# Kernel tuning notes

Hardware: AMD Instinct MI355X
Metric: run time of the kernel (lower is better)

Reference implementation:

```python
import jax, jax.numpy as jnp
import numpy as np

B, T_IN, F, NB = 32768, 3, 6, 10
H = 256
BD = H // 2            # baseline_dim
T_OUT = 5
DIN = F + H + BD       # decoder LSTMCell input size
EPS = 1e-5


def _lstm_cell(x, h, c, W_ih, W_hh, b_ih, b_hh):
    # PyTorch gate order: i, f, g, o
    z = x @ W_ih.T + h @ W_hh.T + b_ih + b_hh
    i, f, g, o = jnp.split(z, 4, axis=-1)
    c = jax.nn.sigmoid(f) * c + jax.nn.sigmoid(i) * jnp.tanh(g)
    h = jax.nn.sigmoid(o) * jnp.tanh(c)
    return h, c


def _lstm_layer(xs, W_ih, W_hh, b_ih, b_hh):
    # xs: (T, B, D_in) -> outputs (T, B, H), final (h, c)
    Bn = xs.shape[1]
    h0 = jnp.zeros((Bn, H), xs.dtype)
    c0 = jnp.zeros((Bn, H), xs.dtype)

    def step(carry, x):
        h, c = carry
        h, c = _lstm_cell(x, h, c, W_ih, W_hh, b_ih, b_hh)
        return (h, c), h

    (hT, cT), ys = jax.lax.scan(step, (h0, c0), xs)
    return ys, hT, cT


def setup_inputs() -> dict:
    key = jax.random.key(0)
    ks = jax.random.split(key, 16)
    s = 0.05
    d = {
        "cbc_input": jax.random.normal(ks[0], (B, T_IN, F), jnp.float32),
        "baseline": jax.random.normal(ks[1], (B, NB), jnp.float32),
        # encoder LSTM layer 0 / 1
        "W_ih0": jax.random.normal(ks[2], (4 * H, F), jnp.float32) * s,
        "W_hh0": jax.random.normal(ks[3], (4 * H, H), jnp.float32) * s,
        "b_ih0": jnp.zeros((4 * H,), jnp.float32),
        "b_hh0": jnp.zeros((4 * H,), jnp.float32),
        "W_ih1": jax.random.normal(ks[4], (4 * H, H), jnp.float32) * s,
        "W_hh1": jax.random.normal(ks[5], (4 * H, H), jnp.float32) * s,
        "b_ih1": jnp.zeros((4 * H,), jnp.float32),
        "b_hh1": jnp.zeros((4 * H,), jnp.float32),
        # baseline encoder: Linear + ReLU + LayerNorm
        "Wb": jax.random.normal(ks[6], (BD, NB), jnp.float32) * s,
        "bb": jnp.zeros((BD,), jnp.float32),
        "ln_g": jnp.ones((BD,), jnp.float32),
        "ln_b": jnp.zeros((BD,), jnp.float32),
        # Bahdanau attention
        "W1a": jax.random.normal(ks[7], (H, H), jnp.float32) * s,
        "b1a": jnp.zeros((H,), jnp.float32),
        "W2a": jax.random.normal(ks[8], (H, H), jnp.float32) * s,
        "b2a": jnp.zeros((H,), jnp.float32),
        "va": jax.random.normal(ks[9], (1, H), jnp.float32) * s,
        "ba": jnp.zeros((1,), jnp.float32),
        # decoder LSTMCell
        "Wd_ih": jax.random.normal(ks[10], (4 * H, DIN), jnp.float32) * s,
        "Wd_hh": jax.random.normal(ks[11], (4 * H, H), jnp.float32) * s,
        "bd_ih": jnp.zeros((4 * H,), jnp.float32),
        "bd_hh": jnp.zeros((4 * H,), jnp.float32),
        # output projection MLP
        "Wo1": jax.random.normal(ks[12], (BD, H), jnp.float32) * s,
        "bo1": jnp.zeros((BD,), jnp.float32),
        "Wo2": jax.random.normal(ks[13], (F, BD), jnp.float32) * s,
        "bo2": jnp.zeros((F,), jnp.float32),
    }
    return d


def reference(cbc_input, baseline, W_ih0, W_hh0, b_ih0, b_hh0,
              W_ih1, W_hh1, b_ih1, b_hh1, Wb, bb, ln_g, ln_b,
              W1a, b1a, W2a, b2a, va, ba,
              Wd_ih, Wd_hh, bd_ih, bd_hh, Wo1, bo1, Wo2, bo2):
    # ---- encoder (2-layer LSTM, batch_first; eval mode so no dropout) ----
    xs = jnp.swapaxes(cbc_input, 0, 1)                      # (T, B, F)
    y0, _, _ = _lstm_layer(xs, W_ih0, W_hh0, b_ih0, b_hh0)  # (T, B, H)
    y1, hT, cT = _lstm_layer(y0, W_ih1, W_hh1, b_ih1, b_hh1)
    encoder_outputs = jnp.swapaxes(y1, 0, 1)                # (B, T, H)

    # ---- baseline encoder: Linear -> ReLU -> LayerNorm ----
    z = jax.nn.relu(baseline @ Wb.T + bb)
    mu = jnp.mean(z, axis=-1, keepdims=True)
    var = jnp.mean((z - mu) ** 2, axis=-1, keepdims=True)
    baseline_repr = (z - mu) * jax.lax.rsqrt(var + EPS) * ln_g + ln_b  # (B, BD)

    enc_proj = encoder_outputs @ W2a.T + b2a                # (B, T, H) precomputed
    last_cbc0 = cbc_input[:, -1, :]                         # (B, F)

    def step(carry, _):
        h, c, last_cbc = carry
        # Bahdanau attention
        q = (h @ W1a.T + b1a)[:, None, :]                   # (B, 1, H)
        scores = jnp.tanh(q + enc_proj) @ va.T + ba         # (B, T, 1)
        weights = jax.nn.softmax(scores, axis=1)
        context = jnp.sum(weights * encoder_outputs, axis=1)  # (B, H)
        dec_in = jnp.concatenate([last_cbc, context, baseline_repr], axis=1)
        h, c = _lstm_cell(dec_in, h, c, Wd_ih, Wd_hh, bd_ih, bd_hh)
        delta = jax.nn.relu(h @ Wo1.T + bo1) @ Wo2.T + bo2
        pred = last_cbc + delta
        return (h, c, pred), pred

    _, preds = jax.lax.scan(step, (hT, cT, last_cbc0), None, length=T_OUT)
    return jnp.swapaxes(preds, 0, 1)                        # (B, 5, F)
```

## Files before the change

### kernel.cpp

```cpp
#include <hip/hip_runtime.h>

typedef unsigned short u16;
typedef __bf16 bf16x8 __attribute__((ext_vector_type(8)));
typedef float f32x4 __attribute__((ext_vector_type(4)));

#define BATCH 32768L

__device__ __forceinline__ u16 f2b(float f) {
  union { float f; unsigned int u; } v; v.f = f;
  unsigned int r = v.u + 0x7fffu + ((v.u >> 16) & 1u);
  return (u16)(r >> 16);
}
__device__ __forceinline__ float b2f(u16 h) {
  union { unsigned int u; float f; } v; v.u = ((unsigned int)h) << 16;
  return v.f;
}
__device__ __forceinline__ float rcpf(float x) { return __builtin_amdgcn_rcpf(x); }
__device__ __forceinline__ float sigf(float x) {
  return rcpf(1.f + __builtin_amdgcn_exp2f(-1.442695041f * x));
}
__device__ __forceinline__ float tanh_f(float x) {
  return 1.f - 2.f * rcpf(1.f + __builtin_amdgcn_exp2f(2.885390082f * x));
}

__device__ __forceinline__ void gload16(const void* g, void* l) {
  __builtin_amdgcn_global_load_lds((const __attribute__((address_space(1))) unsigned int*)g,
                                   (__attribute__((address_space(3))) unsigned int*)l,
                                   16, 0, 0);
}

struct PrepP {
  const float* s[9]; u16* d[9]; int sc[9]; int dc[9]; long n[9];
  const float* ba[3]; const float* bb_[3]; float* bo[3];
};

__global__ void prep_kernel(PrepP p, long cvtTotal, long total) {
  for (long i = (long)blockIdx.x * blockDim.x + threadIdx.x; i < total;
       i += (long)gridDim.x * blockDim.x) {
    if (i < cvtTotal) {
      long off = i; int sg = 0;
      while (off >= p.n[sg]) { off -= p.n[sg]; ++sg; }
      long r = off / p.dc[sg]; int c = (int)(off - r * p.dc[sg]);
      p.d[sg][off] = (c < p.sc[sg]) ? f2b(p.s[sg][r * (long)p.sc[sg] + c]) : (u16)0;
    } else {
      long j = i - cvtTotal; int sg = (int)(j >> 10); int k = (int)(j & 1023);
      p.bo[sg][k] = p.ba[sg][k] + p.bb_[sg][k];
    }
  }
}

template <int EPI, int NG, int REMAP>
__global__ __launch_bounds__(256, 3)
void mfma_gemm7(const u16* __restrict__ A1, long lda1, int K1,
                const u16* __restrict__ W1, int wld1,
                const u16* __restrict__ A2, long lda2, int K2,
                const u16* __restrict__ W2, int wld2,
                int gs, int ys, const float* __restrict__ bias,
                u16* __restrict__ out0, int ldo, int relu,
                const float* __restrict__ cprev, float* __restrict__ cout,
                u16* __restrict__ hout, int ldh)
{
  __shared__ u16 As[2][64 * 32];
  __shared__ u16 Bs[2][NG * 64 * 32];
  const int tid = threadIdx.x;
  const int l = tid & 63, w = tid >> 6;

  int row_blk, yb;
  if constexpr (REMAP) {
    const int vid = blockIdx.x;
    row_blk = (vid >> 5) * 8 + (vid & 7);
    yb = (vid >> 3) & 3;
  } else {
    row_blk = blockIdx.x;
    yb = blockIdx.y;
  }
  const long bm = (long)row_blk * 64;

  const int nch1 = K1 >> 5;
  const int nch2 = A2 ? (K2 >> 5) : 0;
  const int nt = nch1 + nch2;

  const int colb = l & 15, rq = l >> 4;

  f32x4 acc[4][NG];
  {
    float bw[NG];
#pragma unroll
    for (int g = 0; g < NG; ++g) bw[g] = bias[g * gs + yb * ys + w * 16 + colb];
#pragma unroll
    for (int rf = 0; rf < 4; ++rf)
#pragma unroll
      for (int g = 0; g < NG; ++g) acc[rf][g] = (f32x4){bw[g], bw[g], bw[g], bw[g]};
  }

  const int l4q = l >> 2;
  const int swzs = (((l & 3) - (l >> 3)) & 3) * 16;

  const char* pA;
  const char* pB[NG];
  auto initA = [&](const u16* A, long lda) {
    pA = (const char*)A + ((bm + w * 16 + l4q) * lda) * 2 + swzs;
  };
  auto initB = [&](const u16* W, int wld) {
#pragma unroll
    for (int c = 0; c < NG; ++c) {
      const int brow = (w * NG + c) * 16 + l4q;
      const long wrow = (long)(brow >> 6) * gs + (long)yb * ys + (brow & 63);
      pB[c] = (const char*)W + (wrow * (long)wld) * 2 + swzs;
    }
  };
  auto stage = [&](int buf) {
    gload16(pA, &As[buf][(w * 16) * 32]);
    pA += 64;
#pragma unroll
    for (int c = 0; c < NG; ++c) {
      gload16(pB[c], &Bs[buf][((w * NG + c) * 16) * 32]);
      pB[c] += 64;
    }
  };

  initA(A1, lda1);
  initB(W1, wld1);
  stage(0);

  const int rb = l & 15;
  const int koff = ((((l >> 4) + ((l & 15) >> 1)) & 3) * 8);
  int cur = 0;
  for (int ch = 0; ch < nt; ++ch) {
    __syncthreads();
    if (ch + 1 < nt) {
      if (A2 && ch + 1 == nch1) { initA(A2, lda2); initB(W2, wld2); }
      stage(cur ^ 1);
    }
    const u16* Ab = As[cur];
    const u16* Bb = Bs[cur];
    bf16x8 af[4];
#pragma unroll
    for (int rf = 0; rf < 4; ++rf)
      af[rf] = *(const bf16x8*)&Ab[(rf * 16 + rb) * 32 + koff];
#pragma unroll
    for (int g = 0; g < NG; ++g) {
      bf16x8 bfr = *(const bf16x8*)&Bb[(g * 64 + w * 16 + rb) * 32 + koff];
#pragma unroll
      for (int rf = 0; rf < 4; ++rf)
        acc[rf][g] = __builtin_amdgcn_mfma_f32_16x16x32_bf16(af[rf], bfr, acc[rf][g], 0, 0, 0);
    }
    cur ^= 1;
  }

  if constexpr (EPI == 0) {
#pragma unroll
    for (int g = 0; g < NG; ++g) {
      const int wrow = g * gs + yb * ys + w * 16 + colb;
#pragma unroll
      for (int rf = 0; rf < 4; ++rf) {
#pragma unroll
        for (int r = 0; r < 4; ++r) {
          float vv = acc[rf][g][r];
          if (relu) vv = fmaxf(vv, 0.f);
          out0[(bm + rf * 16 + rq * 4 + r) * (long)ldo + wrow] = f2b(vv);
        }
      }
    }
  } else {
    const int cb = yb * ys + w * 16 + colb;
#pragma unroll
    for (int rf = 0; rf < 4; ++rf) {
#pragma unroll
      for (int r = 0; r < 4; ++r) {
        const long row = bm + rf * 16 + rq * 4 + r;
        const float zi = acc[rf][0][r];
        const float zf = acc[rf][1][r];
        const float zg = acc[rf][2][r];
        const float zo = acc[rf][3][r];
        const float cp = cprev ? cprev[row * 256 + cb] : 0.f;
        const float cn = sigf(zf) * cp + sigf(zi) * tanh_f(zg);
        const float hn = sigf(zo) * tanh_f(cn);
        cout[row * 256 + cb] = cn;
        hout[row * (long)ldh + cb] = f2b(hn);
      }
    }
  }
}

__global__ __launch_bounds__(256)
void front_kernel(const float* __restrict__ cbc, const float* __restrict__ baseline,
                  const float* __restrict__ Wb, const float* __restrict__ bb,
                  const float* __restrict__ ln_g, const float* __restrict__ ln_b,
                  u16* __restrict__ dec_in, u16* __restrict__ xbf)
{
  __shared__ float wbs[1280];
  __shared__ float bbs[128], lgs[128], lbs[128];
  const int tid = threadIdx.x;
  for (int i = tid; i < 1280; i += 256) wbs[i] = Wb[i];
  if (tid < 128) { bbs[tid] = bb[tid]; lgs[tid] = ln_g[tid]; lbs[tid] = ln_b[tid]; }
  __syncthreads();
  const int l = tid & 63, w = tid >> 6;
  const long row = (long)blockIdx.x * 4 + w;
#pragma unroll
  for (int e = l; e < 96; e += 64) {
    const int t = e >> 5, c = e & 31;
    xbf[(row * 3 + t) * 32 + c] = (c < 6) ? f2b(cbc[row * 18 + t * 6 + c]) : (u16)0;
  }
  if (l < 6) dec_in[row * 416 + l] = f2b(cbc[row * 18 + 12 + l]);
  else if (l < 32) dec_in[row * 416 + 390 + (l - 6)] = 0;
  float bl[10];
#pragma unroll
  for (int k = 0; k < 10; ++k) bl[k] = baseline[row * 10 + k];
  const int c0 = l, c1 = l + 64;
  float z0 = bbs[c0], z1 = bbs[c1];
#pragma unroll
  for (int k = 0; k < 10; ++k) { z0 += bl[k] * wbs[c0 * 10 + k]; z1 += bl[k] * wbs[c1 * 10 + k]; }
  z0 = fmaxf(z0, 0.f); z1 = fmaxf(z1, 0.f);
  float s = z0 + z1, sq = z0 * z0 + z1 * z1;
#pragma unroll
  for (int m = 32; m; m >>= 1) { s += __shfl_xor(s, m); sq += __shfl_xor(sq, m); }
  const float mu = s * (1.f / 128.f);
  const float var = sq * (1.f / 128.f) - mu * mu;
  const float rs = rsqrtf(var + 1e-5f);
  dec_in[row * 416 + 262 + c0] = f2b((z0 - mu) * rs * lgs[c0] + lbs[c0]);
  dec_in[row * 416 + 262 + c1] = f2b((z1 - mu) * rs * lgs[c1] + lbs[c1]);
}

__global__ __launch_bounds__(256)
void attn_kernel(const u16* __restrict__ q, const u16* __restrict__ ep,
                 const u16* __restrict__ eo, const float* __restrict__ va,
                 const float* __restrict__ ba, u16* __restrict__ dec_in)
{
  const int tid = threadIdx.x;
  const int l = tid & 63, w = tid >> 6;
  const long row = (long)blockIdx.x * 4 + w;
  const int c = l * 4;
  float qv[4], vav[4];
  {
    ushort4 qu = *(const ushort4*)&q[row * 256 + c];
    qv[0] = b2f(qu.x); qv[1] = b2f(qu.y); qv[2] = b2f(qu.z); qv[3] = b2f(qu.w);
    float4 vv = *(const float4*)&va[c];
    vav[0] = vv.x; vav[1] = vv.y; vav[2] = vv.z; vav[3] = vv.w;
  }
  float s[3];
#pragma unroll
  for (int t = 0; t < 3; ++t) {
    ushort4 eu = *(const ushort4*)&ep[row * 768 + t * 256 + c];
    float p = tanh_f(qv[0] + b2f(eu.x)) * vav[0]
            + tanh_f(qv[1] + b2f(eu.y)) * vav[1]
            + tanh_f(qv[2] + b2f(eu.z)) * vav[2]
            + tanh_f(qv[3] + b2f(eu.w)) * vav[3];
#pragma unroll
    for (int m = 32; m; m >>= 1) p += __shfl_xor(p, m);
    s[t] = p + ba[0];
  }
  const float mx = fmaxf(s[0], fmaxf(s[1], s[2]));
  const float e0 = __expf(s[0] - mx), e1 = __expf(s[1] - mx), e2 = __expf(s[2] - mx);
  const float inv = rcpf(e0 + e1 + e2);
  const float w0 = e0 * inv, w1 = e1 * inv, w2 = e2 * inv;
  const ushort4 a0 = *(const ushort4*)&eo[row * 768 + 0 * 256 + c];
  const ushort4 a1 = *(const ushort4*)&eo[row * 768 + 1 * 256 + c];
  const ushort4 a2 = *(const ushort4*)&eo[row * 768 + 2 * 256 + c];
  u16* dp = &dec_in[row * 416 + 6 + c];
  dp[0] = f2b(w0 * b2f(a0.x) + w1 * b2f(a1.x) + w2 * b2f(a2.x));
  dp[1] = f2b(w0 * b2f(a0.y) + w1 * b2f(a1.y) + w2 * b2f(a2.y));
  dp[2] = f2b(w0 * b2f(a0.z) + w1 * b2f(a1.z) + w2 * b2f(a2.z));
  dp[3] = f2b(w0 * b2f(a0.w) + w1 * b2f(a1.w) + w2 * b2f(a2.w));
}

__global__ __launch_bounds__(256)
void delta_kernel(const u16* __restrict__ t1, const float* __restrict__ Wo2,
                  const float* __restrict__ bo2, const float* __restrict__ lastp, int lstride,
                  float* __restrict__ outp, int ostride, u16* __restrict__ dec_in)
{
  __shared__ float w2s[768];
  __shared__ float part[64][4][6];
  const int tid = threadIdx.x;
  for (int i = tid; i < 768; i += 256) w2s[i] = Wo2[i];
  __syncthreads();
  const int rw = tid >> 2, q = tid & 3;
  const long row = (long)blockIdx.x * 64 + rw;
  float p[6] = {0.f, 0.f, 0.f, 0.f, 0.f, 0.f};
  const u16* tp = &t1[row * 128 + q * 32];
#pragma unroll
  for (int it = 0; it < 4; ++it) {
    int4 chunk = *(const int4*)&tp[it * 8];
    const u16* cu = (const u16*)&chunk;
#pragma unroll
    for (int e = 0; e < 8; ++e) {
      const float tv = b2f(cu[e]);
      const int k = q * 32 + it * 8 + e;
#pragma unroll
      for (int j = 0; j < 6; ++j) p[j] += tv * w2s[j * 128 + k];
    }
  }
#pragma unroll
  for (int j = 0; j < 6; ++j) part[rw][q][j] = p[j];
  __syncthreads();
  if (tid < 64) {
    const long r2 = (long)blockIdx.x * 64 + tid;
#pragma unroll
    for (int j = 0; j < 6; ++j) {
      const float d = bo2[j] + part[tid][0][j] + part[tid][1][j] + part[tid][2][j] + part[tid][3][j];
      const float pr = lastp[r2 * lstride + j] + d;
      outp[r2 * ostride + j] = pr;
      dec_in[r2 * 416 + j] = f2b(pr);
    }
  }
}

extern "C" void kernel_launch(void* const* d_in, const int* in_sizes, int n_in,
                              void* d_out, int out_size, void* d_ws, size_t ws_size,
                              hipStream_t stream) {
  const float* cbc   = (const float*)d_in[0];
  const float* base  = (const float*)d_in[1];
  const float* W_ih0 = (const float*)d_in[2];
  const float* W_hh0 = (const float*)d_in[3];
  const float* b_ih0 = (const float*)d_in[4];
  const float* b_hh0 = (const float*)d_in[5];
  const float* W_ih1 = (const float*)d_in[6];
  const float* W_hh1 = (const float*)d_in[7];
  const float* b_ih1 = (const float*)d_in[8];
  const float* b_hh1 = (const float*)d_in[9];
  const float* Wb    = (const float*)d_in[10];
  const float* bb    = (const float*)d_in[11];
  const float* ln_g  = (const float*)d_in[12];
  const float* ln_b  = (const float*)d_in[13];
  const float* W1a   = (const float*)d_in[14];
  const float* b1a   = (const float*)d_in[15];
  const float* W2a   = (const float*)d_in[16];
  const float* b2a   = (const float*)d_in[17];
  const float* va    = (const float*)d_in[18];
  const float* ba    = (const float*)d_in[19];
  const float* Wd_ih = (const float*)d_in[20];
  const float* Wd_hh = (const float*)d_in[21];
  const float* bd_ih = (const float*)d_in[22];
  const float* bd_hh = (const float*)d_in[23];
  const float* Wo1   = (const float*)d_in[24];
  const float* bo1   = (const float*)d_in[25];
  const float* Wo2   = (const float*)d_in[26];
  const float* bo2   = (const float*)d_in[27];
  float* out = (float*)d_out;
  (void)in_sizes; (void)n_in; (void)out_size;

  unsigned char* wsb = (unsigned char*)d_ws;
  size_t off = 0;
  auto alloc = [&](size_t bytes) -> void* {
    void* p = wsb + off;
    off += (bytes + 255) & ~(size_t)255;
    return p;
  };
  u16* wih0b = (u16*)alloc(1024 * 32 * 2);
  u16* whh0b = (u16*)alloc(1024 * 256 * 2);
  u16* wih1b = (u16*)alloc(1024 * 256 * 2);
  u16* whh1b = (u16*)alloc(1024 * 256 * 2);
  u16* wdihb = (u16*)alloc(1024 * 416 * 2);
  u16* wdhhb = (u16*)alloc(1024 * 256 * 2);
  u16* w1ab  = (u16*)alloc(256 * 256 * 2);
  u16* w2ab  = (u16*)alloc(256 * 256 * 2);
  u16* wo1b  = (u16*)alloc(128 * 256 * 2);
  float* bsum0 = (float*)alloc(1024 * 4);
  float* bsum1 = (float*)alloc(1024 * 4);
  float* bsumd = (float*)alloc(1024 * 4);

  const long perRow = 6656;
  long avail = (long)ws_size - (long)off - 32768;
  long R = avail > 0 ? avail / perRow : 512;
  R &= ~511L;
  if (R > BATCH) R = BATCH;
  if (R < 512) R = 512;

  u16* xbf    = (u16*)alloc((size_t)R * 96 * 2);
  u16* y0     = (u16*)alloc((size_t)R * 768 * 2);
  u16* y1     = (u16*)alloc((size_t)R * 768 * 2);
  float* cbuf = (float*)alloc((size_t)R * 256 * 4);
  u16* hdec0  = (u16*)alloc((size_t)R * 256 * 2);
  u16* hdec1  = (u16*)alloc((size_t)R * 256 * 2);
  u16* qt1    = (u16*)alloc((size_t)R * 256 * 2);
  u16* dec_in = (u16*)alloc((size_t)R * 416 * 2);

  {
    PrepP p;
    const float* ss[9] = {W_ih0, W_hh0, W_ih1, W_hh1, Wd_ih, Wd_hh, W1a, W2a, Wo1};
    u16* dd[9]         = {wih0b, whh0b, wih1b, whh1b, wdihb, wdhhb, w1ab, w2ab, wo1b};
    int scv[9]         = {6, 256, 256, 256, 390, 256, 256, 256, 256};
    int dcv[9]         = {32, 256, 256, 256, 416, 256, 256, 256, 256};
    long rows[9]       = {1024, 1024, 1024, 1024, 1024, 1024, 256, 256, 128};
    long cvtTotal = 0;
    for (int i = 0; i < 9; ++i) {
      p.s[i] = ss[i]; p.d[i] = dd[i]; p.sc[i] = scv[i]; p.dc[i] = dcv[i];
      p.n[i] = rows[i] * dcv[i]; cvtTotal += p.n[i];
    }
    p.ba[0] = b_ih0; p.bb_[0] = b_hh0; p.bo[0] = bsum0;
    p.ba[1] = b_ih1; p.bb_[1] = b_hh1; p.bo[1] = bsum1;
    p.ba[2] = bd_ih; p.bb_[2] = bd_hh; p.bo[2] = bsumd;
    prep_kernel<<<dim3(2048), dim3(256), 0, stream>>>(p, cvtTotal, cvtTotal + 3072);
  }

  const dim3 blk(256);

  for (long r0 = 0; r0 < BATCH; r0 += R) {
    const long Rc = (BATCH - r0 < R) ? (BATCH - r0) : R;
    const unsigned nb = (unsigned)(Rc / 64);
    const dim3 gcell(nb * 4);
    const float* cbc_c  = cbc + r0 * 18;
    const float* base_c = base + r0 * 10;
    float* out_c = out + r0 * 30;

    front_kernel<<<dim3((unsigned)(Rc / 4)), blk, 0, stream>>>(
        cbc_c, base_c, Wb, bb, ln_g, ln_b, dec_in, xbf);

    for (int t = 0; t < 3; ++t) {
      const u16* a2 = t ? (y0 + (t - 1) * 256) : nullptr;
      mfma_gemm7<1, 4, 1><<<gcell, blk, 0, stream>>>(
          xbf + t * 32, 96, 32, wih0b, 32,
          a2, 768, 256, whh0b, 256,
          256, 64, bsum0,
          nullptr, 0, 0,
          (t ? cbuf : nullptr), cbuf, y0 + t * 256, 768);
    }
    for (int t = 0; t < 3; ++t) {
      const u16* a2 = t ? (y1 + (t - 1) * 256) : nullptr;
      mfma_gemm7<1, 4, 1><<<gcell, blk, 0, stream>>>(
          y0 + t * 256, 768, 256, wih1b, 256,
          a2, 768, 256, whh1b, 256,
          256, 64, bsum1,
          nullptr, 0, 0,
          (t ? cbuf : nullptr), cbuf, y1 + t * 256, 768);
    }
    mfma_gemm7<0, 4, 0><<<dim3(nb * 3, 1), blk, 0, stream>>>(
        y1, 256, 256, w2ab, 256,
        nullptr, 0, 0, nullptr, 0,
        64, 0, b2a,
        y0, 256, 0,
        nullptr, nullptr, nullptr, 0);

    const u16* hcur = y1 + 2 * 256; long hld = 768;
    for (int s = 0; s < 5; ++s) {
      mfma_gemm7<0, 4, 0><<<dim3(nb, 1), blk, 0, stream>>>(
          hcur, hld, 256, w1ab, 256,
          nullptr, 0, 0, nullptr, 0,
          64, 0, b1a,
          qt1, 256, 0,
          nullptr, nullptr, nullptr, 0);
      attn_kernel<<<dim3((unsigned)(Rc / 4)), blk, 0, stream>>>(qt1, y0, y1, va, ba, dec_in);
      u16* hnext = (s & 1) ? hdec1 : hdec0;
      mfma_gemm7<1, 4, 1><<<gcell, blk, 0, stream>>>(
          dec_in, 416, 416, wdihb, 416,
          hcur, hld, 256, wdhhb, 256,
          256, 64, bsumd,
          nullptr, 0, 0,
          cbuf, cbuf, hnext, 256);
      hcur = hnext; hld = 256;
      mfma_gemm7<0, 2, 0><<<dim3(nb, 1), blk, 0, stream>>>(
          hcur, 256, 256, wo1b, 256,
          nullptr, 0, 0, nullptr, 0,
          64, 0, bo1,
          qt1, 128, 1,
          nullptr, nullptr, nullptr, 0);
      const float* lastp = (s == 0) ? (cbc_c + 12) : (out_c + (long)(s - 1) * 6);
      const int lstr = (s == 0) ? 18 : 30;
      delta_kernel<<<dim3((unsigned)(Rc / 64)), blk, 0, stream>>>(
          qt1, Wo2, bo2, lastp, lstr, out_c + (long)s * 6, 30, dec_in);
    }
  }
}
```

Before: 927.9 us.

## Deepen GEMM load pipeline with triple-buffered A tiles and partial vmcnt waits

The bf16 MFMA GEMM main loop now triple-buffers the A tile and double-buffers B. The A load is issued two chunks ahead and the B load one chunk ahead. The full __syncthreads is replaced by an explicit s_waitcnt vmcnt(1)/s_barrier, so the most recent A prefetch can stay in flight across the barrier. The MFMA block is also wrapped in s_setprio to favour math issue. Shared memory grows by one A buffer, and correctness now relies on hand-counted outstanding global loads.

Result: slower. 998.5 us (+7.6%).

```diff
diff --git a/kernel.cpp b/kernel.cpp
--- a/kernel.cpp
+++ b/kernel.cpp
@@ -51,7 +51,7 @@
 
 template <int EPI, int NG, int REMAP>
 __global__ __launch_bounds__(256, 3)
-void mfma_gemm7(const u16* __restrict__ A1, long lda1, int K1,
+void mfma_gemm8(const u16* __restrict__ A1, long lda1, int K1,
                 const u16* __restrict__ W1, int wld1,
                 const u16* __restrict__ A2, long lda2, int K2,
                 const u16* __restrict__ W2, int wld2,
@@ -60,7 +60,7 @@
                 const float* __restrict__ cprev, float* __restrict__ cout,
                 u16* __restrict__ hout, int ldh)
 {
-  __shared__ u16 As[2][64 * 32];
+  __shared__ u16 As[3][64 * 32];
   __shared__ u16 Bs[2][NG * 64 * 32];
   const int tid = threadIdx.x;
   const int l = tid & 63, w = tid >> 6;
@@ -109,9 +109,13 @@
       pB[c] = (const char*)W + (wrow * (long)wld) * 2 + swzs;
     }
   };
-  auto stage = [&](int buf) {
+  auto stageA = [&](int s, int buf) {
+    if (A2 && s == nch1) initA(A2, lda2);
     gload16(pA, &As[buf][(w * 16) * 32]);
     pA += 64;
+  };
+  auto stageB = [&](int s, int buf) {
+    if (A2 && s == nch1) initB(W2, wld2);
 #pragma unroll
     for (int c = 0; c < NG; ++c) {
       gload16(pB[c], &Bs[buf][((w * NG + c) * 16) * 32]);
@@ -121,23 +125,31 @@
 
   initA(A1, lda1);
   initB(W1, wld1);
-  stage(0);
+  stageA(0, 0);
+  stageB(0, 0);
+  if (nt > 1) stageA(1, 1);
 
   const int rb = l & 15;
   const int koff = ((((l >> 4) + ((l & 15) >> 1)) & 3) * 8);
-  int cur = 0;
+  int bA = 0, bB = 0;
   for (int ch = 0; ch < nt; ++ch) {
-    __syncthreads();
     if (ch + 1 < nt) {
-      if (A2 && ch + 1 == nch1) { initA(A2, lda2); initB(W2, wld2); }
-      stage(cur ^ 1);
-    }
-    const u16* Ab = As[cur];
-    const u16* Bb = Bs[cur];
+      asm volatile("s_waitcnt vmcnt(1)\n\ts_barrier" ::: "memory");
+    } else {
+      asm volatile("s_waitcnt vmcnt(0)\n\ts_barrier" ::: "memory");
+    }
+    if (ch + 1 < nt) stageB(ch + 1, bB ^ 1);
+    if (ch + 2 < nt) {
+      int nxt = bA + 2; if (nxt >= 3) nxt -= 3;
+      stageA(ch + 2, nxt);
+    }
+    const u16* Ab = As[bA];
+    const u16* Bb = Bs[bB];
     bf16x8 af[4];
 #pragma unroll
     for (int rf = 0; rf < 4; ++rf)
       af[rf] = *(const bf16x8*)&Ab[(rf * 16 + rb) * 32 + koff];
+    __builtin_amdgcn_s_setprio(1);
 #pragma unroll
     for (int g = 0; g < NG; ++g) {
       bf16x8 bfr = *(const bf16x8*)&Bb[(g * 64 + w * 16 + rb) * 32 + koff];
@@ -145,7 +157,9 @@
       for (int rf = 0; rf < 4; ++rf)
         acc[rf][g] = __builtin_amdgcn_mfma_f32_16x16x32_bf16(af[rf], bfr, acc[rf][g], 0, 0, 0);
     }
-    cur ^= 1;
+    __builtin_amdgcn_s_setprio(0);
+    bA = (bA + 1 == 3) ? 0 : bA + 1;
+    bB ^= 1;
   }
 
   if constexpr (EPI == 0) {
@@ -408,7 +422,7 @@
 
     for (int t = 0; t < 3; ++t) {
       const u16* a2 = t ? (y0 + (t - 1) * 256) : nullptr;
-      mfma_gemm7<1, 4, 1><<<gcell, blk, 0, stream>>>(
+      mfma_gemm8<1, 4, 1><<<gcell, blk, 0, stream>>>(
           xbf + t * 32, 96, 32, wih0b, 32,
           a2, 768, 256, whh0b, 256,
           256, 64, bsum0,
@@ -417,14 +431,14 @@
     }
     for (int t = 0; t < 3; ++t) {
       const u16* a2 = t ? (y1 + (t - 1) * 256) : nullptr;
-      mfma_gemm7<1, 4, 1><<<gcell, blk, 0, stream>>>(
+      mfma_gemm8<1, 4, 1><<<gcell, blk, 0, stream>>>(
           y0 + t * 256, 768, 256, wih1b, 256,
           a2, 768, 256, whh1b, 256,
           256, 64, bsum1,
           nullptr, 0, 0,
           (t ? cbuf : nullptr), cbuf, y1 + t * 256, 768);
     }
-    mfma_gemm7<0, 4, 0><<<dim3(nb * 3, 1), blk, 0, stream>>>(
+    mfma_gemm8<0, 4, 0><<<dim3(nb * 3, 1), blk, 0, stream>>>(
         y1, 256, 256, w2ab, 256,
         nullptr, 0, 0, nullptr, 0,
         64, 0, b2a,
@@ -433,7 +447,7 @@
 
     const u16* hcur = y1 + 2 * 256; long hld = 768;
     for (int s = 0; s < 5; ++s) {
-      mfma_gemm7<0, 4, 0><<<dim3(nb, 1), blk, 0, stream>>>(
+      mfma_gemm8<0, 4, 0><<<dim3(nb, 1), blk, 0, stream>>>(
           hcur, hld, 256, w1ab, 256,
           nullptr, 0, 0, nullptr, 0,
           64, 0, b1a,
@@ -441,14 +455,14 @@
           nullptr, nullptr, nullptr, 0);
       attn_kernel<<<dim3((unsigned)(Rc / 4)), blk, 0, stream>>>(qt1, y0, y1, va, ba, dec_in);
       u16* hnext = (s & 1) ? hdec1 : hdec0;
-      mfma_gemm7<1, 4, 1><<<gcell, blk, 0, stream>>>(
+      mfma_gemm8<1, 4, 1><<<gcell, blk, 0, stream>>>(
           dec_in, 416, 416, wdihb, 416,
           hcur, hld, 256, wdhhb, 256,
           256, 64, bsumd,
           nullptr, 0, 0,
           cbuf, cbuf, hnext, 256);
       hcur = hnext; hld = 256;
-      mfma_gemm7<0, 2, 0><<<dim3(nb, 1), blk, 0, stream>>>(
+      mfma_gemm8<0, 2, 0><<<dim3(nb, 1), blk, 0, stream>>>(
           hcur, 256, 256, wo1b, 256,
           nullptr, 0, 0, nullptr, 0,
           64, 0, bo1,
```

## Fuse query GEMM with attention and output MLP with delta in decoder

Applied to the files above, without the earlier changes.

Per decoder step, the W1a query projection GEMM is merged with the attention/softmax/context kernel, and the Wo1 ReLU GEMM is merged with the Wo2 delta/prediction kernel. Each fused kernel keeps its GEMM tile in LDS instead of writing it to global memory and reading it back, and it removes two launches per step. The cell GEMMs also get a templated min-waves launch bound, raised to 4. The cost is larger LDS use per block in the fused kernels, lower occupancy (launch bound of 2), and attention now handles only 64 rows per block with each wave walking 16 rows serially.

Result: faster. 881.6 us (-5.0%).

```diff
diff --git a/kernel.cpp b/kernel.cpp
--- a/kernel.cpp
+++ b/kernel.cpp
@@ -49,8 +49,8 @@
   }
 }
 
-template <int EPI, int NG, int REMAP>
-__global__ __launch_bounds__(256, 3)
+template <int EPI, int NG, int REMAP, int MINW>
+__global__ __launch_bounds__(256, MINW)
 void mfma_gemm7(const u16* __restrict__ A1, long lda1, int K1,
                 const u16* __restrict__ W1, int wld1,
                 const u16* __restrict__ A2, long lda2, int K2,
@@ -179,6 +179,249 @@
         cout[row * 256 + cb] = cn;
         hout[row * (long)ldh + cb] = f2b(hn);
       }
+    }
+  }
+}
+
+__global__ __launch_bounds__(256, 2)
+void qattn_kernel(const u16* __restrict__ A1, long lda1,
+                  const u16* __restrict__ W1, int wld1,
+                  const float* __restrict__ bias,
+                  const u16* __restrict__ ep, const u16* __restrict__ eo,
+                  const float* __restrict__ va, const float* __restrict__ ba,
+                  u16* __restrict__ dec_in)
+{
+  __shared__ u16 As[2][64 * 32];
+  __shared__ u16 Bs[2][4 * 64 * 32];
+  __shared__ u16 qs[64 * 260];
+  const int tid = threadIdx.x;
+  const int l = tid & 63, w = tid >> 6;
+  const long bm = (long)blockIdx.x * 64;
+  const int nt = 8;
+
+  const int colb = l & 15, rq = l >> 4;
+
+  f32x4 acc[4][4];
+  {
+    float bw[4];
+#pragma unroll
+    for (int g = 0; g < 4; ++g) bw[g] = bias[g * 64 + w * 16 + colb];
+#pragma unroll
+    for (int rf = 0; rf < 4; ++rf)
+#pragma unroll
+      for (int g = 0; g < 4; ++g) acc[rf][g] = (f32x4){bw[g], bw[g], bw[g], bw[g]};
+  }
+
+  const int l4q = l >> 2;
+  const int swzs = (((l & 3) - (l >> 3)) & 3) * 16;
+
+  const char* pA = (const char*)A1 + ((bm + w * 16 + l4q) * lda1) * 2 + swzs;
+  const char* pB[4];
+#pragma unroll
+  for (int c = 0; c < 4; ++c) {
+    const int brow = (w * 4 + c) * 16 + l4q;
+    pB[c] = (const char*)W1 + ((long)brow * wld1) * 2 + swzs;
+  }
+  auto stage = [&](int buf) {
+    gload16(pA, &As[buf][(w * 16) * 32]);
+    pA += 64;
+#pragma unroll
+    for (int c = 0; c < 4; ++c) {
+      gload16(pB[c], &Bs[buf][((w * 4 + c) * 16) * 32]);
+      pB[c] += 64;
+    }
+  };
+
+  stage(0);
+  const int rb = l & 15;
+  const int koff = ((((l >> 4) + ((l & 15) >> 1)) & 3) * 8);
+  int cur = 0;
+  for (int ch = 0; ch < nt; ++ch) {
+    __syncthreads();
+    if (ch + 1 < nt) stage(cur ^ 1);
+    const u16* Ab = As[cur];
+    const u16* Bb = Bs[cur];
+    bf16x8 af[4];
+#pragma unroll
+    for (int rf = 0; rf < 4; ++rf)
+      af[rf] = *(const bf16x8*)&Ab[(rf * 16 + rb) * 32 + koff];
+#pragma unroll
+    for (int g = 0; g < 4; ++g) {
+      bf16x8 bfr = *(const bf16x8*)&Bb[(g * 64 + w * 16 + rb) * 32 + koff];
+#pragma unroll
+      for (int rf = 0; rf < 4; ++rf)
+        acc[rf][g] = __builtin_amdgcn_mfma_f32_16x16x32_bf16(af[rf], bfr, acc[rf][g], 0, 0, 0);
+    }
+    cur ^= 1;
+  }
+
+#pragma unroll
+  for (int g = 0; g < 4; ++g) {
+    const int col = g * 64 + w * 16 + colb;
+#pragma unroll
+    for (int rf = 0; rf < 4; ++rf)
+#pragma unroll
+      for (int r = 0; r < 4; ++r)
+        qs[(rf * 16 + rq * 4 + r) * 260 + col] = f2b(acc[rf][g][r]);
+  }
+  __syncthreads();
+
+  const float ba0 = ba[0];
+  const int c = l * 4;
+  float vav[4];
+  {
+    float4 vv = *(const float4*)&va[c];
+    vav[0] = vv.x; vav[1] = vv.y; vav[2] = vv.z; vav[3] = vv.w;
+  }
+  for (int rr = 0; rr < 16; ++rr) {
+    const int lrow = w * 16 + rr;
+    const long row = bm + lrow;
+    float qv[4];
+    {
+      ushort4 qu = *(const ushort4*)&qs[lrow * 260 + c];
+      qv[0] = b2f(qu.x); qv[1] = b2f(qu.y); qv[2] = b2f(qu.z); qv[3] = b2f(qu.w);
+    }
+    float s[3];
+#pragma unroll
+    for (int t = 0; t < 3; ++t) {
+      ushort4 eu = *(const ushort4*)&ep[row * 768 + t * 256 + c];
+      float p = tanh_f(qv[0] + b2f(eu.x)) * vav[0]
+              + tanh_f(qv[1] + b2f(eu.y)) * vav[1]
+              + tanh_f(qv[2] + b2f(eu.z)) * vav[2]
+              + tanh_f(qv[3] + b2f(eu.w)) * vav[3];
+#pragma unroll
+      for (int m = 32; m; m >>= 1) p += __shfl_xor(p, m);
+      s[t] = p + ba0;
+    }
+    const float mx = fmaxf(s[0], fmaxf(s[1], s[2]));
+    const float e0 = __expf(s[0] - mx), e1 = __expf(s[1] - mx), e2 = __expf(s[2] - mx);
+    const float inv = rcpf(e0 + e1 + e2);
+    const float w0 = e0 * inv, w1 = e1 * inv, w2 = e2 * inv;
+    const ushort4 a0 = *(const ushort4*)&eo[row * 768 + 0 * 256 + c];
+    const ushort4 a1 = *(const ushort4*)&eo[row * 768 + 1 * 256 + c];
+    const ushort4 a2 = *(const ushort4*)&eo[row * 768 + 2 * 256 + c];
+    u16* dp = &dec_in[row * 416 + 6 + c];
+    dp[0] = f2b(w0 * b2f(a0.x) + w1 * b2f(a1.x) + w2 * b2f(a2.x));
+    dp[1] = f2b(w0 * b2f(a0.y) + w1 * b2f(a1.y) + w2 * b2f(a2.y));
+    dp[2] = f2b(w0 * b2f(a0.z) + w1 * b2f(a1.z) + w2 * b2f(a2.z));
+    dp[3] = f2b(w0 * b2f(a0.w) + w1 * b2f(a1.w) + w2 * b2f(a2.w));
+  }
+}
+
+__global__ __launch_bounds__(256, 2)
+void t1delta_kernel(const u16* __restrict__ A1, long lda1,
+                    const u16* __restrict__ W1, int wld1,
+                    const float* __restrict__ bias,
+                    const float* __restrict__ Wo2, const float* __restrict__ bo2,
+                    const float* __restrict__ lastp, int lstride,
+                    float* __restrict__ outp, int ostride,
+                    u16* __restrict__ dec_in)
+{
+  __shared__ u16 As[2][64 * 32];
+  __shared__ u16 Bs[2][2 * 64 * 32];
+  __shared__ u16 t1s[64 * 136];
+  __shared__ float w2s[768];
+  __shared__ float part[64][4][6];
+  const int tid = threadIdx.x;
+  const int l = tid & 63, w = tid >> 6;
+  const long bm = (long)blockIdx.x * 64;
+  const int nt = 8;
+
+  for (int i = tid; i < 768; i += 256) w2s[i] = Wo2[i];
+
+  const int colb = l & 15, rq = l >> 4;
+
+  f32x4 acc[4][2];
+  {
+    float bw[2];
+#pragma unroll
+    for (int g = 0; g < 2; ++g) bw[g] = bias[g * 64 + w * 16 + colb];
+#pragma unroll
+    for (int rf = 0; rf < 4; ++rf)
+#pragma unroll
+      for (int g = 0; g < 2; ++g) acc[rf][g] = (f32x4){bw[g], bw[g], bw[g], bw[g]};
+  }
+
+  const int l4q = l >> 2;
+  const int swzs = (((l & 3) - (l >> 3)) & 3) * 16;
+
+  const char* pA = (const char*)A1 + ((bm + w * 16 + l4q) * lda1) * 2 + swzs;
+  const char* pB[2];
+#pragma unroll
+  for (int c = 0; c < 2; ++c) {
+    const int brow = (w * 2 + c) * 16 + l4q;
+    pB[c] = (const char*)W1 + ((long)brow * wld1) * 2 + swzs;
+  }
+  auto stage = [&](int buf) {
+    gload16(pA, &As[buf][(w * 16) * 32]);
+    pA += 64;
+#pragma unroll
+    for (int c = 0; c < 2; ++c) {
+      gload16(pB[c], &Bs[buf][((w * 2 + c) * 16) * 32]);
+      pB[c] += 64;
+    }
+  };
+
+  stage(0);
+  const int rb = l & 15;
+  const int koff = ((((l >> 4) + ((l & 15) >> 1)) & 3) * 8);
+  int cur = 0;
+  for (int ch = 0; ch < nt; ++ch) {
+    __syncthreads();
+    if (ch + 1 < nt) stage(cur ^ 1);
+    const u16* Ab = As[cur];
+    const u16* Bb = Bs[cur];
+    bf16x8 af[4];
+#pragma unroll
+    for (int rf = 0; rf < 4; ++rf)
+      af[rf] = *(const bf16x8*)&Ab[(rf * 16 + rb) * 32 + koff];
+#pragma unroll
+    for (int g = 0; g < 2; ++g) {
+      bf16x8 bfr = *(const bf16x8*)&Bb[(g * 64 + w * 16 + rb) * 32 + koff];
+#pragma unroll
+      for (int rf = 0; rf < 4; ++rf)
+        acc[rf][g] = __builtin_amdgcn_mfma_f32_16x16x32_bf16(af[rf], bfr, acc[rf][g], 0, 0, 0);
+    }
+    cur ^= 1;
+  }
+
+#pragma unroll
+  for (int g = 0; g < 2; ++g) {
+    const int col = g * 64 + w * 16 + colb;
+#pragma unroll
+    for (int rf = 0; rf < 4; ++rf)
+#pragma unroll
+      for (int r = 0; r < 4; ++r)
+        t1s[(rf * 16 + rq * 4 + r) * 136 + col] = f2b(fmaxf(acc[rf][g][r], 0.f));
+  }
+  __syncthreads();
+
+  const int rw = tid >> 2, q = tid & 3;
+  float p[6] = {0.f, 0.f, 0.f, 0.f, 0.f, 0.f};
+  const u16* tp = &t1s[rw * 136 + q * 32];
+#pragma unroll
+  for (int it = 0; it < 4; ++it) {
+    int4 chunk = *(const int4*)&tp[it * 8];
+    const u16* cu = (const u16*)&chunk;
+#pragma unroll
+    for (int e = 0; e < 8; ++e) {
+      const float tv = b2f(cu[e]);
+      const int k = q * 32 + it * 8 + e;
+#pragma unroll
+      for (int j = 0; j < 6; ++j) p[j] += tv * w2s[j * 128 + k];
+    }
+  }
+#pragma unroll
+  for (int j = 0; j < 6; ++j) part[rw][q][j] = p[j];
+  __syncthreads();
+  if (tid < 64) {
+    const long r2 = bm + tid;
+#pragma unroll
+    for (int j = 0; j < 6; ++j) {
+      const float d = bo2[j] + part[tid][0][j] + part[tid][1][j] + part[tid][2][j] + part[tid][3][j];
+      const float pr = lastp[r2 * lstride + j] + d;
+      outp[r2 * ostride + j] = pr;
+      dec_in[r2 * 416 + j] = f2b(pr);
     }
   }
 }
@@ -220,89 +463,6 @@
   const float rs = rsqrtf(var + 1e-5f);
   dec_in[row * 416 + 262 + c0] = f2b((z0 - mu) * rs * lgs[c0] + lbs[c0]);
   dec_in[row * 416 + 262 + c1] = f2b((z1 - mu) * rs * lgs[c1] + lbs[c1]);
-}
-
-__global__ __launch_bounds__(256)
-void attn_kernel(const u16* __restrict__ q, const u16* __restrict__ ep,
-                 const u16* __restrict__ eo, const float* __restrict__ va,
-                 const float* __restrict__ ba, u16* __restrict__ dec_in)
-{
-  const int tid = threadIdx.x;
-  const int l = tid & 63, w = tid >> 6;
-  const long row = (long)blockIdx.x * 4 + w;
-  const int c = l * 4;
-  float qv[4], vav[4];
-  {
-    ushort4 qu = *(const ushort4*)&q[row * 256 + c];
-    qv[0] = b2f(qu.x); qv[1] = b2f(qu.y); qv[2] = b2f(qu.z); qv[3] = b2f(qu.w);
-    float4 vv = *(const float4*)&va[c];
-    vav[0] = vv.x; vav[1] = vv.y; vav[2] = vv.z; vav[3] = vv.w;
-  }
-  float s[3];
-#pragma unroll
-  for (int t = 0; t < 3; ++t) {
-    ushort4 eu = *(const ushort4*)&ep[row * 768 + t * 256 + c];
-    float p = tanh_f(qv[0] + b2f(eu.x)) * vav[0]
-            + tanh_f(qv[1] + b2f(eu.y)) * vav[1]
-            + tanh_f(qv[2] + b2f(eu.z)) * vav[2]
-            + tanh_f(qv[3] + b2f(eu.w)) * vav[3];
-#pragma unroll
-    for (int m = 32; m; m >>= 1) p += __shfl_xor(p, m);
-    s[t] = p + ba[0];
-  }
-  const float mx = fmaxf(s[0], fmaxf(s[1], s[2]));
-  const float e0 = __expf(s[0] - mx), e1 = __expf(s[1] - mx), e2 = __expf(s[2] - mx);
-  const float inv = rcpf(e0 + e1 + e2);
-  const float w0 = e0 * inv, w1 = e1 * inv, w2 = e2 * inv;
-  const ushort4 a0 = *(const ushort4*)&eo[row * 768 + 0 * 256 + c];
-  const ushort4 a1 = *(const ushort4*)&eo[row * 768 + 1 * 256 + c];
-  const ushort4 a2 = *(const ushort4*)&eo[row * 768 + 2 * 256 + c];
-  u16* dp = &dec_in[row * 416 + 6 + c];
-  dp[0] = f2b(w0 * b2f(a0.x) + w1 * b2f(a1.x) + w2 * b2f(a2.x));
-  dp[1] = f2b(w0 * b2f(a0.y) + w1 * b2f(a1.y) + w2 * b2f(a2.y));
-  dp[2] = f2b(w0 * b2f(a0.z) + w1 * b2f(a1.z) + w2 * b2f(a2.z));
-  dp[3] = f2b(w0 * b2f(a0.w) + w1 * b2f(a1.w) + w2 * b2f(a2.w));
-}
-
-__global__ __launch_bounds__(256)
-void delta_kernel(const u16* __restrict__ t1, const float* __restrict__ Wo2,
-                  const float* __restrict__ bo2, const float* __restrict__ lastp, int lstride,
-                  float* __restrict__ outp, int ostride, u16* __restrict__ dec_in)
-{
-  __shared__ float w2s[768];
-  __shared__ float part[64][4][6];
-  const int tid = threadIdx.x;
-  for (int i = tid; i < 768; i += 256) w2s[i] = Wo2[i];
-  __syncthreads();
-  const int rw = tid >> 2, q = tid & 3;
-  const long row = (long)blockIdx.x * 64 + rw;
-  float p[6] = {0.f, 0.f, 0.f, 0.f, 0.f, 0.f};
-  const u16* tp = &t1[row * 128 + q * 32];
-#pragma unroll
-  for (int it = 0; it < 4; ++it) {
-    int4 chunk = *(const int4*)&tp[it * 8];
-    const u16* cu = (const u16*)&chunk;
-#pragma unroll
-    for (int e = 0; e < 8; ++e) {
-      const float tv = b2f(cu[e]);
-      const int k = q * 32 + it * 8 + e;
-#pragma unroll
-      for (int j = 0; j < 6; ++j) p[j] += tv * w2s[j * 128 + k];
-    }
-  }
-#pragma unroll
-  for (int j = 0; j < 6; ++j) part[rw][q][j] = p[j];
-  __syncthreads();
-  if (tid < 64) {
-    const long r2 = (long)blockIdx.x * 64 + tid;
-#pragma unroll
-    for (int j = 0; j < 6; ++j) {
-      const float d = bo2[j] + part[tid][0][j] + part[tid][1][j] + part[tid][2][j] + part[tid][3][j];
-      const float pr = lastp[r2 * lstride + j] + d;
-      outp[r2 * ostride + j] = pr;
-      dec_in[r2 * 416 + j] = f2b(pr);
-    }
-  }
 }
 
 extern "C" void kernel_launch(void* const* d_in, const int* in_sizes, int n_in,
@@ -374,6 +534,7 @@
   u16* hdec1  = (u16*)alloc((size_t)R * 256 * 2);
   u16* qt1    = (u16*)alloc((size_t)R * 256 * 2);
   u16* dec_in = (u16*)alloc((size_t)R * 416 * 2);
+  (void)qt1;
 
   {
     PrepP p;
@@ -408,7 +569,7 @@
 
     for (int t = 0; t < 3; ++t) {
       const u16* a2 = t ? (y0 + (t - 1) * 256) : nullptr;
-      mfma_gemm7<1, 4, 1><<<gcell, blk, 0, stream>>>(
+      mfma_gemm7<1, 4, 1, 4><<<gcell, blk, 0, stream>>>(
           xbf + t * 32, 96, 32, wih0b, 32,
           a2, 768, 256, whh0b, 256,
           256, 64, bsum0,
@@ -417,14 +578,14 @@
     }
     for (int t = 0; t < 3; ++t) {
       const u16* a2 = t ? (y1 + (t - 1) * 256) : nullptr;
-      mfma_gemm7<1, 4, 1><<<gcell, blk, 0, stream>>>(
+      mfma_gemm7<1, 4, 1, 4><<<gcell, blk, 0, stream>>>(
           y0 + t * 256, 768, 256, wih1b, 256,
           a2, 768, 256, whh1b, 256,
           256, 64, bsum1,
           nullptr, 0, 0,
           (t ? cbuf : nullptr), cbuf, y1 + t * 256, 768);
     }
-    mfma_gemm7<0, 4, 0><<<dim3(nb * 3, 1), blk, 0, stream>>>(
+    mfma_gemm7<0, 4, 0, 3><<<dim3(nb * 3, 1), blk, 0, stream>>>(
         y1, 256, 256, w2ab, 256,
         nullptr, 0, 0, nullptr, 0,
         64, 0, b2a,
@@ -433,31 +594,21 @@
 
     const u16* hcur = y1 + 2 * 256; long hld = 768;
     for (int s = 0; s < 5; ++s) {
-      mfma_gemm7<0, 4, 0><<<dim3(nb, 1), blk, 0, stream>>>(
-          hcur, hld, 256, w1ab, 256,
-          nullptr, 0, 0, nullptr, 0,
-          64, 0, b1a,
-          qt1, 256, 0,
-          nullptr, nullptr, nullptr, 0);
-      attn_kernel<<<dim3((unsigned)(Rc / 4)), blk, 0, stream>>>(qt1, y0, y1, va, ba, dec_in);
+      qattn_kernel<<<dim3(nb), blk, 0, stream>>>(
+          hcur, hld, w1ab, 256, b1a, y0, y1, va, ba, dec_in);
       u16* hnext = (s & 1) ? hdec1 : hdec0;
-      mfma_gemm7<1, 4, 1><<<gcell, blk, 0, stream>>>(
+      mfma_gemm7<1, 4, 1, 4><<<gcell, blk, 0, stream>>>(
           dec_in, 416, 416, wdihb, 416,
           hcur, hld, 256, wdhhb, 256,
           256, 64, bsumd,
           nullptr, 0, 0,
           cbuf, cbuf, hnext, 256);
       hcur = hnext; hld = 256;
-      mfma_gemm7<0, 2, 0><<<dim3(nb, 1), blk, 0, stream>>>(
-          hcur, 256, 256, wo1b, 256,
-          nullptr, 0, 0, nullptr, 0,
-          64, 0, bo1,
-          qt1, 128, 1,
-          nullptr, nullptr, nullptr, 0);
       const float* lastp = (s == 0) ? (cbc_c + 12) : (out_c + (long)(s - 1) * 6);
       const int lstr = (s == 0) ? 18 : 30;
-      delta_kernel<<<dim3((unsigned)(Rc / 64)), blk, 0, stream>>>(
-          qt1, Wo2, bo2, lastp, lstr, out_c + (long)s * 6, 30, dec_in);
-    }
-  }
-}
+      t1delta_kernel<<<dim3(nb), blk, 0, stream>>>(
+          hcur, 256, wo1b, 256, bo1,
+          Wo2, bo2, lastp, lstr, out_c + (long)s * 6, 30, dec_in);
+    }
+  }
+}
```
